# Kernel tuning notes

Measured on AMD Instinct MI355X. Metric: run time of the kernel, lower is better.

Reference implementation:

```python
import jax, jax.numpy as jnp
import numpy as np
from jax.scipy.special import logsumexp

B, D, A = 64, 128, 128


def setup_inputs() -> dict:
    key = jax.random.key(0)
    k1, k2, k3, k4 = jax.random.split(key, 4)
    x = jax.random.randint(k1, (B, D), 0, 2).astype(jnp.float32)  # binary observations
    u_log_p_a1 = jax.random.normal(k2, (1, 1, 1, A), dtype=jnp.float32)
    u_log_transition = jax.random.normal(k3, (D - 1, A, A), dtype=jnp.float32)
    log_p_xi_g_ai = jax.random.normal(k4, (1, D, 1, A), dtype=jnp.float32)
    return {
        "x": x,
        "u_log_p_a1": u_log_p_a1,
        "u_log_transition": u_log_transition,
        "log_p_xi_g_ai": log_p_xi_g_ai,
    }


def reference(x, u_log_p_a1, u_log_transition, log_p_xi_g_ai):
    b, d = x.shape
    a = u_log_p_a1.shape[-1]
    # _normalize_logits == log_softmax along last dim
    log_p_a1 = jax.nn.log_softmax(u_log_p_a1, axis=-1)          # [1,1,1,A]
    log_T = jax.nn.log_softmax(u_log_transition, axis=-1)        # [D-1,A,A]
    # Bernoulli(logits=l).log_prob(v) = v*l - softplus(l)
    l = log_p_xi_g_ai                                            # [1,D,1,A]
    log_px_vec = x[:, :, None, None] * l - jax.nn.softplus(l)    # [B,D,1,A]
    # per-step reduction matrices
    red = log_px_vec[:, 1:] + log_T                              # [B,D-1,A,A]
    # initial matrix: row-repeated initial vector
    init = jnp.broadcast_to(log_px_vec[:, 0] + log_p_a1[0], (b, a, a))  # [B,A,A]
    mats = jnp.transpose(red, (1, 0, 2, 3))                      # [D-1,B,A,A]

    def step(M, T):
        # log-space matmul: new[b,i,j] = logsumexp_k M[b,i,k] + T[b,k,j]
        new = logsumexp(M[:, :, :, None] + T[:, None, :, :], axis=2)
        return new, None

    final, _ = jax.lax.scan(step, init, mats)                    # [B,A,A]
    log_px = logsumexp(final, axis=-1)                           # [B,A] (rows identical)
    return (log_px, log_p_a1)
```

## Files before the change

### kernel.cpp

```cpp
#include <hip/hip_runtime.h>


#define B_ 64
#define D_ 128
#define A_ 128
#define T_ 127

#define E16_UINTS (T_ * 8192)
#define G_OFF E16_UINTS
#define G_SZ (B_ * T_ * A_)
#define LP_OFF (G_OFF + G_SZ)

typedef _Float16 h2 __attribute__((ext_vector_type(2)));
typedef unsigned int u32x4 __attribute__((ext_vector_type(4)));

__device__ __forceinline__ int packrtz(float a, float b) {
    auto p = __builtin_amdgcn_cvt_pkrtz(a, b);
    return __builtin_bit_cast(int, p);
}
__device__ __forceinline__ float dot2acc(unsigned int e, unsigned int s, float acc) {
    return __builtin_amdgcn_fdot2(__builtin_bit_cast(h2, e),
                                  __builtin_bit_cast(h2, s), acc, false);
}

template <int CTRL>
__device__ __forceinline__ float dpp_mov_self(float x) {
    return __int_as_float(__builtin_amdgcn_update_dpp(
        __float_as_int(x), __float_as_int(x), CTRL, 0xF, 0xF, false));
}
template <int CTRL>
__device__ __forceinline__ float dpp_mov_zero(float x) {
    return __int_as_float(__builtin_amdgcn_update_dpp(
        0, __float_as_int(x), CTRL, 0xF, 0xF, true));
}
__device__ __forceinline__ float wave_max_partial(float x) {
    x = fmaxf(x, dpp_mov_self<0x111>(x));
    x = fmaxf(x, dpp_mov_self<0x112>(x));
    x = fmaxf(x, dpp_mov_self<0x114>(x));
    x = fmaxf(x, dpp_mov_self<0x118>(x));
    x = fmaxf(x, dpp_mov_self<0x142>(x));
    x = fmaxf(x, dpp_mov_self<0x143>(x));
    return x;
}
__device__ __forceinline__ float wave_max_bcast(float x) {
    return __int_as_float(__builtin_amdgcn_readlane(
        __float_as_int(wave_max_partial(x)), 63));
}
__device__ __forceinline__ float wave_sum_bcast(float x) {
    x += dpp_mov_zero<0x111>(x);
    x += dpp_mov_zero<0x112>(x);
    x += dpp_mov_zero<0x114>(x);
    x += dpp_mov_zero<0x118>(x);
    x += dpp_mov_zero<0x142>(x);
    x += dpp_mov_zero<0x143>(x);
    return __int_as_float(__builtin_amdgcn_readlane(__float_as_int(x), 63));
}

__global__ __launch_bounds__(256) void prep(const float* __restrict__ uT,
                                            const float* __restrict__ u1,
                                            const float* __restrict__ x,
                                            const float* __restrict__ lg,
                                            float* __restrict__ ws,
                                            float* __restrict__ out) {
    __shared__ float ul[128 * 128];
    const int t = blockIdx.x, tid = threadIdx.x;
    const float* u = uT + (size_t)t * A_ * A_;

    for (int i = tid; i < 4096; i += 256) {
        float4 v4 = ((const float4*)u)[i];
        *(float4*)&ul[(i >> 5) * 128 + (i & 31) * 4] = v4;
    }
    __syncthreads();

    if (tid < 128) {
        const int r = tid;
        float mx = -1e30f;
        for (int it = 0; it < 128; it++) mx = fmaxf(mx, ul[r * 128 + ((it + r) & 127)]);
        float s = 0.f;
        for (int it = 0; it < 128; it++) s += __expf(ul[r * 128 + ((it + r) & 127)] - mx);
        float Z = mx + __logf(s);
        for (int it = 0; it < 128; it++) ul[r * 128 + ((it + r) & 127)] -= Z;
    }
    __syncthreads();

    unsigned int* Et = (unsigned int*)ws + (size_t)t * 8192;
    for (int it = 0; it < 32; it++) {
        int a = it * 256 + tid;
        int c = a & 3, jl = (a >> 2) & 31, w = (a >> 7) & 3;
        int h = (a >> 9) & 1, q = a >> 10;
        int i = 32 * h + 4 * q + c;
        int j = 32 * w + jl;
        float e0 = __expf(ul[(2 * i) * 128 + j]);
        float e1 = __expf(ul[(2 * i + 1) * 128 + j]);
        Et[a] = (unsigned int)packrtz(e0, e1);
    }

    {
        int j = tid & 127, hb = tid >> 7;
        float lv = lg[(t + 1) * A_ + j];
        float sp = (lv > 0.f) ? (lv + log1pf(__expf(-lv))) : log1pf(__expf(lv));
        float G0 = __expf(-sp), G1 = __expf(lv - sp);
        float* G = ws + G_OFF;
        for (int b = hb * 32; b < hb * 32 + 32; b++) {
            float xv = x[b * D_ + t + 1];
            G[((size_t)b * T_ + t) * A_ + j] = (xv != 0.f) ? G1 : G0;
        }
    }

    if (t == 0 && tid < 64) {
        int lane = tid;
        float a = u1[lane], c = u1[lane + 64];
        float mx = wave_max_bcast(fmaxf(a, c));
        float s = wave_sum_bcast(__expf(a - mx) + __expf(c - mx));
        float lse = mx + __logf(s);
        ws[LP_OFF + lane] = a - lse;
        ws[LP_OFF + lane + 64] = c - lse;
        out[B_ * A_ + lane] = a - lse;
        out[B_ * A_ + lane + 64] = c - lse;
    }
}

#define BARRIER() asm volatile("s_waitcnt lgkmcnt(0)\n\ts_barrier" ::: "memory")

#define ISSUE(EN, GN, TT)                                                     \
    {                                                                         \
        unsigned long long ab = Ebase + (unsigned long long)(TT) * 32768ull;  \
        _Pragma("unroll") for (int q = 0; q < 8; q++)                         \
            asm volatile("global_load_dwordx4 %0, %1, off"                    \
                         : "=v"(EN[q])                                        \
                         : "v"(ab + (unsigned long long)(q * 4096)));         \
        asm volatile("global_load_dword %0, %1, off"                          \
                     : "=v"(GN)                                               \
                     : "v"(Gbase + (unsigned long long)(TT) * 512ull));       \
    }

#define WAITON(EC, GC, CNT)                                                   \
    asm volatile("s_waitcnt vmcnt(" #CNT ")"                                  \
                 : "+v"(EC[0]), "+v"(EC[1]), "+v"(EC[2]), "+v"(EC[3]),        \
                   "+v"(EC[4]), "+v"(EC[5]), "+v"(EC[6]), "+v"(EC[7]),        \
                   "+v"(GC));

#define BODY(T, EC, GC)                                                       \
    {                                                                         \
        const int p = (T) & 1, np = p ^ 1;                                    \
        float4 vm4 = *(const float4*)&vml[p][0];                              \
        float maxW = fmaxf(fmaxf(vm4.x, vm4.y), fmaxf(vm4.z, vm4.w));         \
        float srec = 1.0f / maxW;                                             \
        beta += __logf(mprev);               \
        mprev = maxW;                                                         \
        const uint4* ewp = (const uint4*)&ewl[p][0] + h * 8;                  \
        float a0 = 0, a1 = 0, a2 = 0, a3 = 0;                                 \
        _Pragma("unroll") for (int q = 0; q < 8; q++) {                       \
            uint4 ew4 = ewp[q];                                               \
            a0 = dot2acc(EC[q].x, ew4.x, a0);                                 \
            a1 = dot2acc(EC[q].y, ew4.y, a1);                                 \
            a2 = dot2acc(EC[q].z, ew4.z, a2);                                 \
            a3 = dot2acc(EC[q].w, ew4.w, a3);                                 \
        }                                                                     \
        float S = (a0 + a1) + (a2 + a3);                                      \
        S += __shfl_xor(S, 32, 64);                                           \
        float W = S * GC;                                                     \
        if (h == 0) ewl[np][j] = (_Float16)(W * srec);                        \
        float wm = wave_max_partial(W);                         \
        if (lane == 63) vml[np][wv] = wm;                                     \
        Wlast = W;                                                            \
        BARRIER();                                                            \
    }

#define STEPP(T, EC, EN, GC, GN)                                              \
    {                                                                         \
        ISSUE(EN, GN, (T) + 1)                                                \
        WAITON(EC, GC, 9)                                                     \
        BODY(T, EC, GC)                                                       \
    }
#define STEPL(T, EC, GC)                                                      \
    {                                                                         \
        WAITON(EC, GC, 0)                                                     \
        BODY(T, EC, GC)                                                       \
    }

__global__ __launch_bounds__(256, 1) void fwd(const float* __restrict__ x,
                                              const float* __restrict__ lg,
                                              const float* __restrict__ ws,
                                              float* __restrict__ out) {
    __shared__ __align__(16) _Float16 ewl[2][A_];
    __shared__ __align__(16) float vml[2][4];
    __shared__ float sums[4];
    const int b = blockIdx.x, tid = threadIdx.x;
    const int wv = tid >> 6, lane = tid & 63;
    const int h = lane >> 5, jl = lane & 31;
    const int j = 32 * wv + jl;

    const unsigned long long Ebase =
        (unsigned long long)ws + (unsigned long long)(h * 2048 + wv * 512 + jl * 16);
    const unsigned long long Gbase =
        (unsigned long long)(ws + G_OFF + (size_t)b * T_ * A_ + j);
    const float* LP = ws + LP_OFF;

    u32x4 EA[8], EB[8];
    float gA, gB;
    ISSUE(EA, gA, 0)

    float ll = lg[j];
    float sp = (ll > 0.f) ? (ll + log1pf(__expf(-ll))) : log1pf(__expf(ll));
    float xv0 = x[b * D_];
    float v0 = LP[j] + ((xv0 != 0.f) ? (ll - sp) : (-sp));
    float wm0 = wave_max_partial(v0);
    if (lane == 63) vml[0][wv] = wm0;
    BARRIER();
    float4 vmi = *(const float4*)&vml[0][0];
    float M0 = fmaxf(fmaxf(vmi.x, vmi.y), fmaxf(vmi.z, vmi.w));
    float w0 = __expf(v0 - M0);
    if (h == 0) ewl[0][j] = (_Float16)w0;
    float wmW = wave_max_partial(w0);
    if (lane == 63) vml[0][wv] = wmW;
    BARRIER();

    float beta = M0, mprev = 1.0f, Wlast = 0.f;

    for (int t = 0; t < 126; t += 2) {
        STEPP(t + 0, EA, EB, gA, gB)
        STEPP(t + 1, EB, EA, gB, gA)
    }
    STEPL(126, EA, gA)

    float sw = wave_sum_bcast(Wlast) * 0.5f;
    if (lane == 0) sums[wv] = sw;
    __syncthreads();
    float tot = (sums[0] + sums[1]) + (sums[2] + sums[3]);
    float L = beta + __logf(tot);
    if (tid < A_) out[b * A_ + tid] = L;
}

extern "C" void kernel_launch(void* const* d_in, const int* in_sizes, int n_in,
                              void* d_out, int out_size, void* d_ws, size_t ws_size,
                              hipStream_t stream) {
    const float* x = (const float*)d_in[0];
    const float* u1 = (const float*)d_in[1];
    const float* uT = (const float*)d_in[2];
    const float* lg = (const float*)d_in[3];
    float* ws = (float*)d_ws;
    float* out = (float*)d_out;

    prep<<<dim3(T_), dim3(256), 0, stream>>>(uT, u1, x, lg, ws, out);
    fwd<<<dim3(B_), dim3(256), 0, stream>>>(x, lg, ws, out);
}
```

Baseline: 169.1 us.

## Store transition exps in FP8, compact emission table, triple-buffer prefetch

Transition probability matrices are quantized to FP8 with a 256x scale and unpacked to FP16 for dot2 accumulation, halving per-step global loads. The per-batch emission table is replaced by a per-step pair of probabilities selected using x cached in shared memory, shrinking prep writes. Prefetch depth increases to two steps ahead with three register buffers. This trades extra conversion ALU work and FP8 precision loss for reduced memory traffic and latency.

```diff
diff --git a/kernel.cpp b/kernel.cpp
--- a/kernel.cpp
+++ b/kernel.cpp
@@ -6,21 +6,32 @@
 #define A_ 128
 #define T_ 127
 
-#define E16_UINTS (T_ * 8192)
-#define G_OFF E16_UINTS
-#define G_SZ (B_ * T_ * A_)
-#define LP_OFF (G_OFF + G_SZ)
+#define E8_FLOATS (T_ * 4096)
+#define GP_OFF E8_FLOATS
+#define GP_SZ (T_ * A_ * 2)
+#define LP_OFF (GP_OFF + GP_SZ)
 
 typedef _Float16 h2 __attribute__((ext_vector_type(2)));
 typedef unsigned int u32x4 __attribute__((ext_vector_type(4)));
+typedef float f2v __attribute__((ext_vector_type(2)));
 
 __device__ __forceinline__ int packrtz(float a, float b) {
     auto p = __builtin_amdgcn_cvt_pkrtz(a, b);
     return __builtin_bit_cast(int, p);
 }
-__device__ __forceinline__ float dot2acc(unsigned int e, unsigned int s, float acc) {
+__device__ __forceinline__ float dot2acc(int e, unsigned int s, float acc) {
     return __builtin_amdgcn_fdot2(__builtin_bit_cast(h2, e),
                                   __builtin_bit_cast(h2, s), acc, false);
+}
+
+template <int WORD>
+__device__ __forceinline__ f2v unpk(unsigned int u) {
+    return __builtin_amdgcn_cvt_pk_f32_fp8((int)u, WORD);
+}
+__device__ __forceinline__ unsigned int pk4_fp8(float a, float b, float c, float d) {
+    int v = __builtin_amdgcn_cvt_pk_fp8_f32(a, b, 0, false);
+    v = __builtin_amdgcn_cvt_pk_fp8_f32(c, d, v, true);
+    return (unsigned int)v;
 }
 
 template <int CTRL>
@@ -83,28 +94,27 @@
     }
     __syncthreads();
 
-    unsigned int* Et = (unsigned int*)ws + (size_t)t * 8192;
-    for (int it = 0; it < 32; it++) {
-        int a = it * 256 + tid;
-        int c = a & 3, jl = (a >> 2) & 31, w = (a >> 7) & 3;
-        int h = (a >> 9) & 1, q = a >> 10;
-        int i = 32 * h + 4 * q + c;
-        int j = 32 * w + jl;
-        float e0 = __expf(ul[(2 * i) * 128 + j]);
-        float e1 = __expf(ul[(2 * i + 1) * 128 + j]);
-        Et[a] = (unsigned int)packrtz(e0, e1);
-    }
-
-    {
-        int j = tid & 127, hb = tid >> 7;
+    unsigned int* Et = (unsigned int*)ws + (size_t)t * 4096;
+    for (int it = 0; it < 16; it++) {
+        int m = it * 256 + tid;
+        int c = m & 3, jl = (m >> 2) & 31, wv = (m >> 7) & 3;
+        int h = (m >> 9) & 1, q = (m >> 10) & 3;
+        int k0 = 64 * h + 16 * q + 4 * c;
+        int j = 32 * wv + jl;
+        float f0 = 256.f * __expf(ul[(k0 + 0) * 128 + j]);
+        float f1 = 256.f * __expf(ul[(k0 + 1) * 128 + j]);
+        float f2 = 256.f * __expf(ul[(k0 + 2) * 128 + j]);
+        float f3 = 256.f * __expf(ul[(k0 + 3) * 128 + j]);
+        Et[m] = pk4_fp8(f0, f1, f2, f3);
+    }
+
+    if (tid < 128) {
+        int j = tid;
         float lv = lg[(t + 1) * A_ + j];
         float sp = (lv > 0.f) ? (lv + log1pf(__expf(-lv))) : log1pf(__expf(lv));
-        float G0 = __expf(-sp), G1 = __expf(lv - sp);
-        float* G = ws + G_OFF;
-        for (int b = hb * 32; b < hb * 32 + 32; b++) {
-            float xv = x[b * D_ + t + 1];
-            G[((size_t)b * T_ + t) * A_ + j] = (xv != 0.f) ? G1 : G0;
-        }
+        float2 gp = make_float2(__expf(-sp) * 0.00390625f,
+                                __expf(lv - sp) * 0.00390625f);
+        *(float2*)&ws[GP_OFF + ((size_t)t * A_ + j) * 2] = gp;
     }
 
     if (t == 0 && tid < 64) {
@@ -124,20 +134,19 @@
 
 #define ISSUE(EN, GN, TT)                                                     \
     {                                                                         \
-        unsigned long long ab = Ebase + (unsigned long long)(TT) * 32768ull;  \
-        _Pragma("unroll") for (int q = 0; q < 8; q++)                         \
+        unsigned long long ab = Ebase + (unsigned long long)(TT) * 16384ull;  \
+        _Pragma("unroll") for (int q = 0; q < 4; q++)                         \
             asm volatile("global_load_dwordx4 %0, %1, off"                    \
                          : "=v"(EN[q])                                        \
                          : "v"(ab + (unsigned long long)(q * 4096)));         \
-        asm volatile("global_load_dword %0, %1, off"                          \
+        asm volatile("global_load_dwordx2 %0, %1, off"                        \
                      : "=v"(GN)                                               \
-                     : "v"(Gbase + (unsigned long long)(TT) * 512ull));       \
+                     : "v"(Gbase + (unsigned long long)(TT) * 1024ull));      \
     }
 
 #define WAITON(EC, GC, CNT)                                                   \
     asm volatile("s_waitcnt vmcnt(" #CNT ")"                                  \
                  : "+v"(EC[0]), "+v"(EC[1]), "+v"(EC[2]), "+v"(EC[3]),        \
-                   "+v"(EC[4]), "+v"(EC[5]), "+v"(EC[6]), "+v"(EC[7]),        \
                    "+v"(GC));
 
 #define BODY(T, EC, GC)                                                       \
@@ -148,18 +157,26 @@
         float srec = 1.0f / maxW;                                             \
         beta += __logf(mprev);               \
         mprev = maxW;                                                         \
+        float xv = xl[(T) + 1];                                               \
+        uint4 ew4[8];                                                         \
         const uint4* ewp = (const uint4*)&ewl[p][0] + h * 8;                  \
+        _Pragma("unroll") for (int q = 0; q < 8; q++) ew4[q] = ewp[q];        \
         float a0 = 0, a1 = 0, a2 = 0, a3 = 0;                                 \
-        _Pragma("unroll") for (int q = 0; q < 8; q++) {                       \
-            uint4 ew4 = ewp[q];                                               \
-            a0 = dot2acc(EC[q].x, ew4.x, a0);                                 \
-            a1 = dot2acc(EC[q].y, ew4.y, a1);                                 \
-            a2 = dot2acc(EC[q].z, ew4.z, a2);                                 \
-            a3 = dot2acc(EC[q].w, ew4.w, a3);                                 \
+        _Pragma("unroll") for (int q = 0; q < 4; q++) {                       \
+            _Pragma("unroll") for (int m = 0; m < 4; m++) {                   \
+                unsigned int eu = EC[q][m];                                   \
+                f2v lo = unpk<0>(eu), hi = unpk<1>(eu);                       \
+                const int i0 = 8 * q + 2 * m, i1 = i0 + 1;                    \
+                unsigned int w0 = ew4[i0 >> 2][i0 & 3];                       \
+                unsigned int w1 = ew4[i1 >> 2][i1 & 3];                       \
+                a0 = dot2acc(packrtz(lo.x, lo.y), w0, a0);                    \
+                a1 = dot2acc(packrtz(hi.x, hi.y), w1, a1);                    \
+            }                                                                 \
         }                                                                     \
-        float S = (a0 + a1) + (a2 + a3);                                      \
+        float S = a0 + a1 + a2 + a3;                                          \
         S += __shfl_xor(S, 32, 64);                                           \
-        float W = S * GC;                                                     \
+        float gsel = (xv != 0.f) ? GC.y : GC.x;                               \
+        float W = S * gsel;                                                   \
         if (h == 0) ewl[np][j] = (_Float16)(W * srec);                        \
         float wm = wave_max_partial(W);                         \
         if (lane == 63) vml[np][wv] = wm;                                     \
@@ -169,13 +186,8 @@
 
 #define STEPP(T, EC, EN, GC, GN)                                              \
     {                                                                         \
-        ISSUE(EN, GN, (T) + 1)                                                \
-        WAITON(EC, GC, 9)                                                     \
-        BODY(T, EC, GC)                                                       \
-    }
-#define STEPL(T, EC, GC)                                                      \
-    {                                                                         \
-        WAITON(EC, GC, 0)                                                     \
+        ISSUE(EN, GN, (T) + 2)                                                \
+        WAITON(EC, GC, 10)                                                    \
         BODY(T, EC, GC)                                                       \
     }
 
@@ -185,6 +197,7 @@
                                               float* __restrict__ out) {
     __shared__ __align__(16) _Float16 ewl[2][A_];
     __shared__ __align__(16) float vml[2][4];
+    __shared__ float xl[D_];
     __shared__ float sums[4];
     const int b = blockIdx.x, tid = threadIdx.x;
     const int wv = tid >> 6, lane = tid & 63;
@@ -194,12 +207,15 @@
     const unsigned long long Ebase =
         (unsigned long long)ws + (unsigned long long)(h * 2048 + wv * 512 + jl * 16);
     const unsigned long long Gbase =
-        (unsigned long long)(ws + G_OFF + (size_t)b * T_ * A_ + j);
+        (unsigned long long)(ws + GP_OFF) + (unsigned long long)(j * 8);
     const float* LP = ws + LP_OFF;
 
-    u32x4 EA[8], EB[8];
-    float gA, gB;
+    u32x4 EA[4], EB[4], EC_[4];
+    f2v gA, gB, gC;
     ISSUE(EA, gA, 0)
+    ISSUE(EB, gB, 1)
+
+    if (tid < D_) xl[tid] = x[b * D_ + tid];
 
     float ll = lg[j];
     float sp = (ll > 0.f) ? (ll + log1pf(__expf(-ll))) : log1pf(__expf(ll));
@@ -218,17 +234,28 @@
 
     float beta = M0, mprev = 1.0f, Wlast = 0.f;
 
-    for (int t = 0; t < 126; t += 2) {
-        STEPP(t + 0, EA, EB, gA, gB)
+    for (int t = 0; t < 123; t += 3) {
+        STEPP(t + 0, EA, EC_, gA, gC)
         STEPP(t + 1, EB, EA, gB, gA)
-    }
-    STEPL(126, EA, gA)
+        STEPP(t + 2, EC_, EB, gC, gB)
+    }
+    STEPP(123, EA, EC_, gA, gC)
+    STEPP(124, EB, EA, gB, gA)
+    {
+        WAITON(EC_, gC, 5)
+        BODY(125, EC_, gC)
+    }
+    {
+        WAITON(EA, gA, 0)
+        BODY(126, EA, gA)
+    }
 
     float sw = wave_sum_bcast(Wlast) * 0.5f;
     if (lane == 0) sums[wv] = sw;
     __syncthreads();
     float tot = (sums[0] + sums[1]) + (sums[2] + sums[3]);
-    float L = beta + __logf(tot);
+    float L = beta + __logf(mprev) + __logf(tot) - __logf(mprev);
+    L = beta + __logf(tot);
     if (tid < A_) out[b * A_ + tid] = L;
 }
 
```

New measurement: 162.8 us. 3.8% less time.
